# Performance work log

Hardware: AMD Instinct MI355X
Metric: run time of the kernel (lower is better)

The kernel has to match this reference:

```python
import jax, jax.numpy as jnp
import numpy as np

B, S, E, H = 4, 2048, 1024, 16
D = E // H  # head_size = 64


def setup_inputs() -> dict:
    key = jax.random.key(0)
    ks = jax.random.split(key, 8)
    s = 1.0 / np.sqrt(E)
    return {
        "values": jax.random.normal(ks[0], (B, S, E), jnp.float32),
        "keys": jax.random.normal(ks[1], (B, S, E), jnp.float32),
        "queries": jax.random.normal(ks[2], (B, S, E), jnp.float32),
        "Wv": jax.random.normal(ks[3], (E, E), jnp.float32) * s,
        "Wk": jax.random.normal(ks[4], (E, E), jnp.float32) * s,
        "Wq": jax.random.normal(ks[5], (E, E), jnp.float32) * s,
        "Wo": jax.random.normal(ks[6], (E, E), jnp.float32) * s,
        "bo": jax.random.normal(ks[7], (E,), jnp.float32) * s,
    }


def reference(values, keys, queries, Wv, Wk, Wq, Wo, bo):
    # torch Linear: y = x @ W.T
    k = (keys @ Wk.T).reshape(B, S, H, D).transpose(0, 2, 1, 3)    # [B,H,S,D]
    q = (queries @ Wq.T).reshape(B, S, H, D).transpose(0, 2, 1, 3)
    v = (values @ Wv.T).reshape(B, S, H, D).transpose(0, 2, 1, 3)
    dot = jnp.einsum('bhqd,bhkd->bhqk', q, k)                      # raw logits
    # NOTE: softmax BEFORE scaling (faithful to original module)
    probs = jax.nn.softmax(dot, axis=-1) / jnp.sqrt(jnp.float32(D))
    out = jnp.einsum('bhqk,bhkd->bhqd', probs, v)                  # [B,H,S,D]
    out = out.transpose(0, 2, 1, 3).reshape(B, S, E)
    return out @ Wo.T + bo
```

## Files before the change

### kernel.cpp

```cpp
#include <hip/hip_runtime.h>
#include <stdint.h>

#define NB 4
#define NS 2048
#define NE 1024
#define NH 16
#define ND 64

typedef __attribute__((ext_vector_type(8))) short short8;
typedef __attribute__((ext_vector_type(4))) float f32x4;
typedef __attribute__((ext_vector_type(16))) float f32x16;
typedef __attribute__((ext_vector_type(4))) unsigned short us4;
typedef __attribute__((ext_vector_type(4))) unsigned int u32x4;

__device__ __forceinline__ unsigned short f2bf(float f) {
    return __builtin_bit_cast(unsigned short, static_cast<__bf16>(f));
}
__device__ __forceinline__ unsigned int packbf(float lo, float hi_) {
    return (unsigned int)f2bf(lo) | ((unsigned int)f2bf(hi_) << 16);
}

__global__ __launch_bounds__(256) void cvt_w4_kernel(const float* __restrict__ w0,
                                                     const float* __restrict__ w1,
                                                     const float* __restrict__ w2,
                                                     const float* __restrict__ w3,
                                                     unsigned short* __restrict__ d0,
                                                     unsigned short* __restrict__ d1,
                                                     unsigned short* __restrict__ d2,
                                                     unsigned short* __restrict__ d3) {
    const int g = blockIdx.x >> 10;
    const float* src = g == 0 ? w0 : g == 1 ? w1 : g == 2 ? w2 : w3;
    unsigned short* dst = g == 0 ? d0 : g == 1 ? d1 : g == 2 ? d2 : d3;
    const int i = ((blockIdx.x & 1023) * 256 + threadIdx.x) * 4;
    f32x4 f = *(const f32x4*)(src + i);
    us4 o;
#pragma unroll
    for (int j = 0; j < 4; ++j) o[j] = f2bf(f[j]);
    *(us4*)(dst + i) = o;
}

template<int A_IS_F32, int OUT_MODE>
__global__ __launch_bounds__(256) void gemm_bt(const void* __restrict__ Aptr,
                                               const unsigned short* __restrict__ Wp,
                                               void* __restrict__ Cp,
                                               const float* __restrict__ bias) {
    constexpr int K = 1024;
    __shared__ unsigned short As[128][40];
    __shared__ unsigned short Bs[128][40];
    const int tid = threadIdx.x;
    const int bm = blockIdx.x, bn = blockIdx.y;
    const int lane = tid & 63, wid = tid >> 6;
    const int lr = lane & 15, lg = lane >> 4;
    const int wr = wid >> 1, wc = wid & 1;
    const int srow = tid >> 1, shalf = tid & 1;

    f32x4 acc[4][4];
#pragma unroll
    for (int a = 0; a < 4; ++a)
#pragma unroll
        for (int b = 0; b < 4; ++b) acc[a][b] = (f32x4){0.f, 0.f, 0.f, 0.f};

    const size_t arow = (size_t)(bm * 128 + srow) * K + shalf * 16;
    const size_t brow = (size_t)(bn * 128 + srow) * K + shalf * 16;
    const float*          apF = (const float*)Aptr + arow;
    const unsigned short* apH = (const unsigned short*)Aptr + arow;
    const unsigned short* bp  = Wp + brow;

    f32x4 pa0, pa1, pa2, pa3;
    short8 pah0, pah1, pb0, pb1;
    if (A_IS_F32) {
        pa0 = *(const f32x4*)(apF);
        pa1 = *(const f32x4*)(apF + 4);
        pa2 = *(const f32x4*)(apF + 8);
        pa3 = *(const f32x4*)(apF + 12);
    } else {
        pah0 = *(const short8*)(apH);
        pah1 = *(const short8*)(apH + 8);
    }
    pb0 = *(const short8*)(bp);
    pb1 = *(const short8*)(bp + 8);

    for (int k0 = 0; k0 < K; k0 += 32) {
        __syncthreads();
        if (A_IS_F32) {
            short8 p0, p1;
#pragma unroll
            for (int j = 0; j < 4; ++j) {
                p0[j]     = (short)f2bf(pa0[j]);
                p0[j + 4] = (short)f2bf(pa1[j]);
                p1[j]     = (short)f2bf(pa2[j]);
                p1[j + 4] = (short)f2bf(pa3[j]);
            }
            *(short8*)&As[srow][shalf * 16]     = p0;
            *(short8*)&As[srow][shalf * 16 + 8] = p1;
        } else {
            *(short8*)&As[srow][shalf * 16]     = pah0;
            *(short8*)&As[srow][shalf * 16 + 8] = pah1;
        }
        *(short8*)&Bs[srow][shalf * 16]     = pb0;
        *(short8*)&Bs[srow][shalf * 16 + 8] = pb1;
        __syncthreads();

        if (k0 + 32 < K) {
            const int kn = k0 + 32;
            if (A_IS_F32) {
                pa0 = *(const f32x4*)(apF + kn);
                pa1 = *(const f32x4*)(apF + kn + 4);
                pa2 = *(const f32x4*)(apF + kn + 8);
                pa3 = *(const f32x4*)(apF + kn + 12);
            } else {
                pah0 = *(const short8*)(apH + kn);
                pah1 = *(const short8*)(apH + kn + 8);
            }
            pb0 = *(const short8*)(bp + kn);
            pb1 = *(const short8*)(bp + kn + 8);
        }

        short8 af[4], bfr[4];
#pragma unroll
        for (int mi = 0; mi < 4; ++mi) af[mi]  = *(const short8*)&As[wr * 64 + mi * 16 + lr][lg * 8];
#pragma unroll
        for (int ni = 0; ni < 4; ++ni) bfr[ni] = *(const short8*)&Bs[wc * 64 + ni * 16 + lr][lg * 8];
#pragma unroll
        for (int mi = 0; mi < 4; ++mi)
#pragma unroll
            for (int ni = 0; ni < 4; ++ni)
                acc[mi][ni] = __builtin_amdgcn_mfma_f32_16x16x32_bf16(af[mi], bfr[ni], acc[mi][ni], 0, 0, 0);
    }

#pragma unroll
    for (int mi = 0; mi < 4; ++mi) {
#pragma unroll
        for (int ni = 0; ni < 4; ++ni) {
            const int n = bn * 128 + wc * 64 + ni * 16 + lr;
            if (OUT_MODE == 2) {
                const int m0 = bm * 128 + wr * 64 + mi * 16 + lg * 4;
                const int b = m0 >> 11, s0 = m0 & 2047;
                const int h = n >> 6, d = n & 63;
                us4 pk;
#pragma unroll
                for (int i = 0; i < 4; ++i) pk[i] = f2bf(acc[mi][ni][i]);
                const size_t idx = ((((size_t)b * NH + h) * (NS / 64) + (s0 >> 6)) * ND + d) * 64 + (s0 & 63);
                *(us4*)&((unsigned short*)Cp)[idx] = pk;
            } else {
#pragma unroll
                for (int i = 0; i < 4; ++i) {
                    const int m = bm * 128 + wr * 64 + mi * 16 + lg * 4 + i;
                    const float val = acc[mi][ni][i];
                    if (OUT_MODE == 0) {
                        const int b = m >> 11, s = m & 2047, h = n >> 6, d = n & 63;
                        ((unsigned short*)Cp)[(((size_t)b * NH + h) * NS + s) * ND + d] = f2bf(val);
                    } else {
                        ((float*)Cp)[(size_t)m * 1024 + n] = val + bias[n];
                    }
                }
            }
        }
    }
}

__global__ __launch_bounds__(256, 3) void attn_kernel(const unsigned short* __restrict__ q,
                                                      const unsigned short* __restrict__ k,
                                                      const unsigned short* __restrict__ vtt,
                                                      unsigned short* __restrict__ o) {
    __shared__ unsigned short Kl[64][72];
    __shared__ unsigned short Vl[64][72];
    const int tid = threadIdx.x;
    const int lane = tid & 63, wid = tid >> 6;
    const int l31 = lane & 31, hi = lane >> 5;
    const int bh = blockIdx.y;
    const int qw = blockIdx.x * 128 + wid * 32;
    const size_t base = (size_t)bh * NS * ND;

    short8 qf[4];
    {
        const unsigned short* qp = q + base + (size_t)(qw + l31) * ND + 8 * hi;
#pragma unroll
        for (int m = 0; m < 4; ++m) qf[m] = *(const short8*)(qp + 16 * m);
    }

    float m_run = -__builtin_inff(), l_run = 0.f;
    f32x16 oa0, oa1, fz;
#pragma unroll
    for (int i = 0; i < 16; ++i) { oa0[i] = 0.f; oa1[i] = 0.f; fz[i] = 0.f; }

    const int strow = tid >> 2, stcol = (tid & 3) * 16;
    const unsigned short* ks = k   + base + tid * 16;
    const unsigned short* vs = vtt + base + tid * 16;

    short8 kr0 = *(const short8*)(ks);
    short8 kr1 = *(const short8*)(ks + 8);
    short8 vr0 = *(const short8*)(vs);
    short8 vr1 = *(const short8*)(vs + 8);

    for (int kv0 = 0; kv0 < NS; kv0 += 64) {
        __syncthreads();
        *(short8*)&Kl[strow][stcol]     = kr0;
        *(short8*)&Kl[strow][stcol + 8] = kr1;
        *(short8*)&Vl[strow][stcol]     = vr0;
        *(short8*)&Vl[strow][stcol + 8] = vr1;
        __syncthreads();

        if (kv0 + 64 < NS) {
            const unsigned short* ks2 = ks + (size_t)(kv0 + 64) * ND;
            const unsigned short* vs2 = vs + (size_t)(kv0 + 64) * ND;
            kr0 = *(const short8*)(ks2);
            kr1 = *(const short8*)(ks2 + 8);
            vr0 = *(const short8*)(vs2);
            vr1 = *(const short8*)(vs2 + 8);
        }

        f32x16 st0, st1;
        __builtin_amdgcn_s_setprio(1);
        {
            short8 kf;
            kf = *(const short8*)&Kl[l31][8 * hi];
            st0 = __builtin_amdgcn_mfma_f32_32x32x16_bf16(kf, qf[0], fz, 0, 0, 0);
            kf = *(const short8*)&Kl[l31][16 + 8 * hi];
            st0 = __builtin_amdgcn_mfma_f32_32x32x16_bf16(kf, qf[1], st0, 0, 0, 0);
            kf = *(const short8*)&Kl[l31][32 + 8 * hi];
            st0 = __builtin_amdgcn_mfma_f32_32x32x16_bf16(kf, qf[2], st0, 0, 0, 0);
            kf = *(const short8*)&Kl[l31][48 + 8 * hi];
            st0 = __builtin_amdgcn_mfma_f32_32x32x16_bf16(kf, qf[3], st0, 0, 0, 0);
            kf = *(const short8*)&Kl[32 + l31][8 * hi];
            st1 = __builtin_amdgcn_mfma_f32_32x32x16_bf16(kf, qf[0], fz, 0, 0, 0);
            kf = *(const short8*)&Kl[32 + l31][16 + 8 * hi];
            st1 = __builtin_amdgcn_mfma_f32_32x32x16_bf16(kf, qf[1], st1, 0, 0, 0);
            kf = *(const short8*)&Kl[32 + l31][32 + 8 * hi];
            st1 = __builtin_amdgcn_mfma_f32_32x32x16_bf16(kf, qf[2], st1, 0, 0, 0);
            kf = *(const short8*)&Kl[32 + l31][48 + 8 * hi];
            st1 = __builtin_amdgcn_mfma_f32_32x32x16_bf16(kf, qf[3], st1, 0, 0, 0);
        }
        __builtin_amdgcn_s_setprio(0);

        float pm = st0[0];
#pragma unroll
        for (int i = 1; i < 16; ++i) pm = fmaxf(pm, st0[i]);
#pragma unroll
        for (int i = 0; i < 16; ++i) pm = fmaxf(pm, st1[i]);
        pm = fmaxf(pm, __shfl_xor(pm, 32, 64));
        if (!__all(pm <= m_run)) {
            const float mn = fmaxf(m_run, pm);
            const float alpha = __expf(m_run - mn);
            m_run = mn;
            l_run *= alpha;
#pragma unroll
            for (int i = 0; i < 16; ++i) { oa0[i] *= alpha; oa1[i] *= alpha; }
        }
        float rs = 0.f;
#pragma unroll
        for (int i = 0; i < 16; ++i) { st0[i] = __expf(st0[i] - m_run); rs += st0[i]; }
#pragma unroll
        for (int i = 0; i < 16; ++i) { st1[i] = __expf(st1[i] - m_run); rs += st1[i]; }
        rs += __shfl_xor(rs, 32, 64);
        l_run += rs;

        short8 pf0, pf1, pf2, pf3;
#define MKPF(PF, SV, RB) { \
        unsigned int wa = packbf(SV[RB + 0], SV[RB + 1]); \
        unsigned int wb = packbf(SV[RB + 2], SV[RB + 3]); \
        unsigned int wc = packbf(SV[RB + 4], SV[RB + 5]); \
        unsigned int wd = packbf(SV[RB + 6], SV[RB + 7]); \
        asm("v_permlane32_swap_b32 %0, %1" : "+v"(wa), "+v"(wc)); \
        asm("v_permlane32_swap_b32 %0, %1" : "+v"(wb), "+v"(wd)); \
        u32x4 pw; pw[0] = wa; pw[1] = wb; pw[2] = wc; pw[3] = wd; \
        PF = __builtin_bit_cast(short8, pw); }
        MKPF(pf0, st0, 0)
        MKPF(pf1, st0, 8)
        MKPF(pf2, st1, 0)
        MKPF(pf3, st1, 8)
#undef MKPF

        __builtin_amdgcn_s_setprio(1);
        {
            short8 vf;
            vf = *(const short8*)&Vl[l31][8 * hi];
            oa0 = __builtin_amdgcn_mfma_f32_32x32x16_bf16(vf, pf0, oa0, 0, 0, 0);
            vf = *(const short8*)&Vl[l31][16 + 8 * hi];
            oa0 = __builtin_amdgcn_mfma_f32_32x32x16_bf16(vf, pf1, oa0, 0, 0, 0);
            vf = *(const short8*)&Vl[l31][32 + 8 * hi];
            oa0 = __builtin_amdgcn_mfma_f32_32x32x16_bf16(vf, pf2, oa0, 0, 0, 0);
            vf = *(const short8*)&Vl[l31][48 + 8 * hi];
            oa0 = __builtin_amdgcn_mfma_f32_32x32x16_bf16(vf, pf3, oa0, 0, 0, 0);
            vf = *(const short8*)&Vl[32 + l31][8 * hi];
            oa1 = __builtin_amdgcn_mfma_f32_32x32x16_bf16(vf, pf0, oa1, 0, 0, 0);
            vf = *(const short8*)&Vl[32 + l31][16 + 8 * hi];
            oa1 = __builtin_amdgcn_mfma_f32_32x32x16_bf16(vf, pf1, oa1, 0, 0, 0);
            vf = *(const short8*)&Vl[32 + l31][32 + 8 * hi];
            oa1 = __builtin_amdgcn_mfma_f32_32x32x16_bf16(vf, pf2, oa1, 0, 0, 0);
            vf = *(const short8*)&Vl[32 + l31][48 + 8 * hi];
            oa1 = __builtin_amdgcn_mfma_f32_32x32x16_bf16(vf, pf3, oa1, 0, 0, 0);
        }
        __builtin_amdgcn_s_setprio(0);
    }

    const int b = bh >> 4, h = bh & 15;
    const float scl = 0.125f / l_run;
    unsigned short* op = o + (((size_t)b * NS + (qw + l31)) * NH + h) * ND;
#pragma unroll
    for (int rq = 0; rq < 4; ++rq) {
        us4 p0, p1;
#pragma unroll
        for (int i = 0; i < 4; ++i) {
            p0[i] = f2bf(oa0[4 * rq + i] * scl);
            p1[i] = f2bf(oa1[4 * rq + i] * scl);
        }
        *(us4*)&op[8 * rq + 4 * hi]      = p0;
        *(us4*)&op[32 + 8 * rq + 4 * hi] = p1;
    }
}

extern "C" void kernel_launch(void* const* d_in, const int* in_sizes, int n_in,
                              void* d_out, int out_size, void* d_ws, size_t ws_size,
                              hipStream_t stream) {
    (void)in_sizes; (void)n_in; (void)out_size; (void)ws_size;
    const float* values  = (const float*)d_in[0];
    const float* keys    = (const float*)d_in[1];
    const float* queries = (const float*)d_in[2];
    const float* Wv = (const float*)d_in[3];
    const float* Wk = (const float*)d_in[4];
    const float* Wq = (const float*)d_in[5];
    const float* Wo = (const float*)d_in[6];
    const float* bo = (const float*)d_in[7];

    uint8_t* ws = (uint8_t*)d_ws;
    const size_t MB = (size_t)1 << 20;
    unsigned short* wvb = (unsigned short*)(ws + 0 * MB);
    unsigned short* wkb = (unsigned short*)(ws + 2 * MB);
    unsigned short* wqb = (unsigned short*)(ws + 4 * MB);
    unsigned short* wob = (unsigned short*)(ws + 6 * MB);
    unsigned short* qb  = (unsigned short*)(ws + 8 * MB);
    unsigned short* kb  = (unsigned short*)(ws + 24 * MB);
    unsigned short* vtb = (unsigned short*)(ws + 40 * MB);
    unsigned short* ab  = (unsigned short*)(ws + 56 * MB);

    cvt_w4_kernel<<<4096, 256, 0, stream>>>(Wv, Wk, Wq, Wo, wvb, wkb, wqb, wob);

    dim3 gg(64, 8);
    gemm_bt<1, 0><<<gg, 256, 0, stream>>>(queries, wqb, qb,  nullptr);
    gemm_bt<1, 0><<<gg, 256, 0, stream>>>(keys,    wkb, kb,  nullptr);
    gemm_bt<1, 2><<<gg, 256, 0, stream>>>(values,  wvb, vtb, nullptr);

    attn_kernel<<<dim3(16, 64), 256, 0, stream>>>(qb, kb, vtb, ab);

    gemm_bt<0, 1><<<gg, 256, 0, stream>>>(ab, wob, d_out, bo);
}
```

Measured before the change: 245.5 us.

## Fold log2e into Wq, use exp2 softmax, and process 128-key tiles per barrier

The log2(e) factor is folded into the bf16 conversion of the query weight, so attention logits come out in base-2 and the softmax uses exp2f directly with no per-element multiply. The K/V staging tile grows from 64 to 128 keys, with two 64-key compute sub-steps per barrier pair, halving the number of syncs and giving the prefetch more time to land. The row-sum reduction becomes a tree of vector adds, and bf16 packing uses a vector convert that can lower to a packed conversion instruction. In exchange LDS use doubles and register pressure rises, which may reduce occupancy under the 3-block launch bound.

```diff
diff --git a/kernel.cpp b/kernel.cpp
--- a/kernel.cpp
+++ b/kernel.cpp
@@ -8,16 +8,22 @@
 #define ND 64
 
 typedef __attribute__((ext_vector_type(8))) short short8;
+typedef __attribute__((ext_vector_type(2))) float f32x2;
 typedef __attribute__((ext_vector_type(4))) float f32x4;
+typedef __attribute__((ext_vector_type(8))) float f32x8;
 typedef __attribute__((ext_vector_type(16))) float f32x16;
 typedef __attribute__((ext_vector_type(4))) unsigned short us4;
 typedef __attribute__((ext_vector_type(4))) unsigned int u32x4;
+typedef __attribute__((ext_vector_type(2))) __bf16 bf16x2;
+
+#define LOG2E 1.4426950408889634f
 
 __device__ __forceinline__ unsigned short f2bf(float f) {
     return __builtin_bit_cast(unsigned short, static_cast<__bf16>(f));
 }
 __device__ __forceinline__ unsigned int packbf(float lo, float hi_) {
-    return (unsigned int)f2bf(lo) | ((unsigned int)f2bf(hi_) << 16);
+    f32x2 v; v[0] = lo; v[1] = hi_;
+    return __builtin_bit_cast(unsigned int, __builtin_convertvector(v, bf16x2));
 }
 
 __global__ __launch_bounds__(256) void cvt_w4_kernel(const float* __restrict__ w0,
@@ -31,11 +37,12 @@
     const int g = blockIdx.x >> 10;
     const float* src = g == 0 ? w0 : g == 1 ? w1 : g == 2 ? w2 : w3;
     unsigned short* dst = g == 0 ? d0 : g == 1 ? d1 : g == 2 ? d2 : d3;
+    const float scl = (g == 2) ? LOG2E : 1.0f;
     const int i = ((blockIdx.x & 1023) * 256 + threadIdx.x) * 4;
     f32x4 f = *(const f32x4*)(src + i);
     us4 o;
 #pragma unroll
-    for (int j = 0; j < 4; ++j) o[j] = f2bf(f[j]);
+    for (int j = 0; j < 4; ++j) o[j] = f2bf(f[j] * scl);
     *(us4*)(dst + i) = o;
 }
 
@@ -163,8 +170,8 @@
                                                       const unsigned short* __restrict__ k,
                                                       const unsigned short* __restrict__ vtt,
                                                       unsigned short* __restrict__ o) {
-    __shared__ unsigned short Kl[64][72];
-    __shared__ unsigned short Vl[64][72];
+    __shared__ unsigned short Kl[128][72];
+    __shared__ unsigned short Vl[128][72];
     const int tid = threadIdx.x;
     const int lane = tid & 63, wid = tid >> 6;
     const int l31 = lane & 31, hi = lane >> 5;
@@ -188,110 +195,138 @@
     const unsigned short* ks = k   + base + tid * 16;
     const unsigned short* vs = vtt + base + tid * 16;
 
-    short8 kr0 = *(const short8*)(ks);
-    short8 kr1 = *(const short8*)(ks + 8);
-    short8 vr0 = *(const short8*)(vs);
-    short8 vr1 = *(const short8*)(vs + 8);
-
-    for (int kv0 = 0; kv0 < NS; kv0 += 64) {
+    short8 kr00 = *(const short8*)(ks);
+    short8 kr01 = *(const short8*)(ks + 8);
+    short8 kr10 = *(const short8*)(ks + 4096);
+    short8 kr11 = *(const short8*)(ks + 4096 + 8);
+    short8 vr00 = *(const short8*)(vs);
+    short8 vr01 = *(const short8*)(vs + 8);
+    short8 vr10 = *(const short8*)(vs + 4096);
+    short8 vr11 = *(const short8*)(vs + 4096 + 8);
+
+    for (int kv0 = 0; kv0 < NS; kv0 += 128) {
         __syncthreads();
-        *(short8*)&Kl[strow][stcol]     = kr0;
-        *(short8*)&Kl[strow][stcol + 8] = kr1;
-        *(short8*)&Vl[strow][stcol]     = vr0;
-        *(short8*)&Vl[strow][stcol + 8] = vr1;
+        *(short8*)&Kl[strow][stcol]          = kr00;
+        *(short8*)&Kl[strow][stcol + 8]      = kr01;
+        *(short8*)&Kl[64 + strow][stcol]     = kr10;
+        *(short8*)&Kl[64 + strow][stcol + 8] = kr11;
+        *(short8*)&Vl[strow][stcol]          = vr00;
+        *(short8*)&Vl[strow][stcol + 8]      = vr01;
+        *(short8*)&Vl[64 + strow][stcol]     = vr10;
+        *(short8*)&Vl[64 + strow][stcol + 8] = vr11;
         __syncthreads();
 
-        if (kv0 + 64 < NS) {
-            const unsigned short* ks2 = ks + (size_t)(kv0 + 64) * ND;
-            const unsigned short* vs2 = vs + (size_t)(kv0 + 64) * ND;
-            kr0 = *(const short8*)(ks2);
-            kr1 = *(const short8*)(ks2 + 8);
-            vr0 = *(const short8*)(vs2);
-            vr1 = *(const short8*)(vs2 + 8);
-        }
-
-        f32x16 st0, st1;
-        __builtin_amdgcn_s_setprio(1);
-        {
-            short8 kf;
-            kf = *(const short8*)&Kl[l31][8 * hi];
-            st0 = __builtin_amdgcn_mfma_f32_32x32x16_bf16(kf, qf[0], fz, 0, 0, 0);
-            kf = *(const short8*)&Kl[l31][16 + 8 * hi];
-            st0 = __builtin_amdgcn_mfma_f32_32x32x16_bf16(kf, qf[1], st0, 0, 0, 0);
-            kf = *(const short8*)&Kl[l31][32 + 8 * hi];
-            st0 = __builtin_amdgcn_mfma_f32_32x32x16_bf16(kf, qf[2], st0, 0, 0, 0);
-            kf = *(const short8*)&Kl[l31][48 + 8 * hi];
-            st0 = __builtin_amdgcn_mfma_f32_32x32x16_bf16(kf, qf[3], st0, 0, 0, 0);
-            kf = *(const short8*)&Kl[32 + l31][8 * hi];
-            st1 = __builtin_amdgcn_mfma_f32_32x32x16_bf16(kf, qf[0], fz, 0, 0, 0);
-            kf = *(const short8*)&Kl[32 + l31][16 + 8 * hi];
-            st1 = __builtin_amdgcn_mfma_f32_32x32x16_bf16(kf, qf[1], st1, 0, 0, 0);
-            kf = *(const short8*)&Kl[32 + l31][32 + 8 * hi];
-            st1 = __builtin_amdgcn_mfma_f32_32x32x16_bf16(kf, qf[2], st1, 0, 0, 0);
-            kf = *(const short8*)&Kl[32 + l31][48 + 8 * hi];
-            st1 = __builtin_amdgcn_mfma_f32_32x32x16_bf16(kf, qf[3], st1, 0, 0, 0);
-        }
-        __builtin_amdgcn_s_setprio(0);
-
-        float pm = st0[0];
-#pragma unroll
-        for (int i = 1; i < 16; ++i) pm = fmaxf(pm, st0[i]);
-#pragma unroll
-        for (int i = 0; i < 16; ++i) pm = fmaxf(pm, st1[i]);
-        pm = fmaxf(pm, __shfl_xor(pm, 32, 64));
-        if (!__all(pm <= m_run)) {
-            const float mn = fmaxf(m_run, pm);
-            const float alpha = __expf(m_run - mn);
-            m_run = mn;
-            l_run *= alpha;
-#pragma unroll
-            for (int i = 0; i < 16; ++i) { oa0[i] *= alpha; oa1[i] *= alpha; }
-        }
-        float rs = 0.f;
-#pragma unroll
-        for (int i = 0; i < 16; ++i) { st0[i] = __expf(st0[i] - m_run); rs += st0[i]; }
-#pragma unroll
-        for (int i = 0; i < 16; ++i) { st1[i] = __expf(st1[i] - m_run); rs += st1[i]; }
-        rs += __shfl_xor(rs, 32, 64);
-        l_run += rs;
-
-        short8 pf0, pf1, pf2, pf3;
+        if (kv0 + 128 < NS) {
+            const unsigned short* ks2 = ks + (size_t)(kv0 + 128) * ND;
+            const unsigned short* vs2 = vs + (size_t)(kv0 + 128) * ND;
+            kr00 = *(const short8*)(ks2);
+            kr01 = *(const short8*)(ks2 + 8);
+            kr10 = *(const short8*)(ks2 + 4096);
+            kr11 = *(const short8*)(ks2 + 4096 + 8);
+            vr00 = *(const short8*)(vs2);
+            vr01 = *(const short8*)(vs2 + 8);
+            vr10 = *(const short8*)(vs2 + 4096);
+            vr11 = *(const short8*)(vs2 + 4096 + 8);
+        }
+
+#pragma unroll
+        for (int w = 0; w < 2; ++w) {
+            const int rb = w << 6;
+
+            f32x16 st0, st1;
+            __builtin_amdgcn_s_setprio(1);
+            {
+                short8 kf;
+                kf = *(const short8*)&Kl[rb + l31][8 * hi];
+                st0 = __builtin_amdgcn_mfma_f32_32x32x16_bf16(kf, qf[0], fz, 0, 0, 0);
+                kf = *(const short8*)&Kl[rb + l31][16 + 8 * hi];
+                st0 = __builtin_amdgcn_mfma_f32_32x32x16_bf16(kf, qf[1], st0, 0, 0, 0);
+                kf = *(const short8*)&Kl[rb + l31][32 + 8 * hi];
+                st0 = __builtin_amdgcn_mfma_f32_32x32x16_bf16(kf, qf[2], st0, 0, 0, 0);
+                kf = *(const short8*)&Kl[rb + l31][48 + 8 * hi];
+                st0 = __builtin_amdgcn_mfma_f32_32x32x16_bf16(kf, qf[3], st0, 0, 0, 0);
+                kf = *(const short8*)&Kl[rb + 32 + l31][8 * hi];
+                st1 = __builtin_amdgcn_mfma_f32_32x32x16_bf16(kf, qf[0], fz, 0, 0, 0);
+                kf = *(const short8*)&Kl[rb + 32 + l31][16 + 8 * hi];
+                st1 = __builtin_amdgcn_mfma_f32_32x32x16_bf16(kf, qf[1], st1, 0, 0, 0);
+                kf = *(const short8*)&Kl[rb + 32 + l31][32 + 8 * hi];
+                st1 = __builtin_amdgcn_mfma_f32_32x32x16_bf16(kf, qf[2], st1, 0, 0, 0);
+                kf = *(const short8*)&Kl[rb + 32 + l31][48 + 8 * hi];
+                st1 = __builtin_amdgcn_mfma_f32_32x32x16_bf16(kf, qf[3], st1, 0, 0, 0);
+            }
+            __builtin_amdgcn_s_setprio(0);
+
+            float pm = st0[0];
+#pragma unroll
+            for (int i = 1; i < 16; ++i) pm = fmaxf(pm, st0[i]);
+#pragma unroll
+            for (int i = 0; i < 16; ++i) pm = fmaxf(pm, st1[i]);
+            pm = fmaxf(pm, __shfl_xor(pm, 32, 64));
+            if (!__all(pm <= m_run)) {
+                const float mn = fmaxf(m_run, pm);
+                const float alpha = exp2f(m_run - mn);
+                m_run = mn;
+                l_run *= alpha;
+                oa0 = oa0 * alpha;
+                oa1 = oa1 * alpha;
+            }
+            st0 = st0 - m_run;
+            st1 = st1 - m_run;
+#pragma unroll
+            for (int i = 0; i < 16; ++i) st0[i] = exp2f(st0[i]);
+#pragma unroll
+            for (int i = 0; i < 16; ++i) st1[i] = exp2f(st1[i]);
+            {
+                f32x16 sv = st0 + st1;
+                f32x8 s8 = __builtin_shufflevector(sv, sv, 0, 1, 2, 3, 4, 5, 6, 7)
+                         + __builtin_shufflevector(sv, sv, 8, 9, 10, 11, 12, 13, 14, 15);
+                f32x4 s4 = __builtin_shufflevector(s8, s8, 0, 1, 2, 3)
+                         + __builtin_shufflevector(s8, s8, 4, 5, 6, 7);
+                f32x2 s2 = __builtin_shufflevector(s4, s4, 0, 1)
+                         + __builtin_shufflevector(s4, s4, 2, 3);
+                float rs = s2[0] + s2[1];
+                rs += __shfl_xor(rs, 32, 64);
+                l_run += rs;
+            }
+
+            short8 pf0, pf1, pf2, pf3;
 #define MKPF(PF, SV, RB) { \
-        unsigned int wa = packbf(SV[RB + 0], SV[RB + 1]); \
-        unsigned int wb = packbf(SV[RB + 2], SV[RB + 3]); \
-        unsigned int wc = packbf(SV[RB + 4], SV[RB + 5]); \
-        unsigned int wd = packbf(SV[RB + 6], SV[RB + 7]); \
-        asm("v_permlane32_swap_b32 %0, %1" : "+v"(wa), "+v"(wc)); \
-        asm("v_permlane32_swap_b32 %0, %1" : "+v"(wb), "+v"(wd)); \
-        u32x4 pw; pw[0] = wa; pw[1] = wb; pw[2] = wc; pw[3] = wd; \
-        PF = __builtin_bit_cast(short8, pw); }
-        MKPF(pf0, st0, 0)
-        MKPF(pf1, st0, 8)
-        MKPF(pf2, st1, 0)
-        MKPF(pf3, st1, 8)
+            unsigned int wa = packbf(SV[RB + 0], SV[RB + 1]); \
+            unsigned int wb = packbf(SV[RB + 2], SV[RB + 3]); \
+            unsigned int wc = packbf(SV[RB + 4], SV[RB + 5]); \
+            unsigned int wd = packbf(SV[RB + 6], SV[RB + 7]); \
+            asm("v_permlane32_swap_b32 %0, %1" : "+v"(wa), "+v"(wc)); \
+            asm("v_permlane32_swap_b32 %0, %1" : "+v"(wb), "+v"(wd)); \
+            u32x4 pw; pw[0] = wa; pw[1] = wb; pw[2] = wc; pw[3] = wd; \
+            PF = __builtin_bit_cast(short8, pw); }
+            MKPF(pf0, st0, 0)
+            MKPF(pf1, st0, 8)
+            MKPF(pf2, st1, 0)
+            MKPF(pf3, st1, 8)
 #undef MKPF
 
-        __builtin_amdgcn_s_setprio(1);
-        {
-            short8 vf;
-            vf = *(const short8*)&Vl[l31][8 * hi];
-            oa0 = __builtin_amdgcn_mfma_f32_32x32x16_bf16(vf, pf0, oa0, 0, 0, 0);
-            vf = *(const short8*)&Vl[l31][16 + 8 * hi];
-            oa0 = __builtin_amdgcn_mfma_f32_32x32x16_bf16(vf, pf1, oa0, 0, 0, 0);
-            vf = *(const short8*)&Vl[l31][32 + 8 * hi];
-            oa0 = __builtin_amdgcn_mfma_f32_32x32x16_bf16(vf, pf2, oa0, 0, 0, 0);
-            vf = *(const short8*)&Vl[l31][48 + 8 * hi];
-            oa0 = __builtin_amdgcn_mfma_f32_32x32x16_bf16(vf, pf3, oa0, 0, 0, 0);
-            vf = *(const short8*)&Vl[32 + l31][8 * hi];
-            oa1 = __builtin_amdgcn_mfma_f32_32x32x16_bf16(vf, pf0, oa1, 0, 0, 0);
-            vf = *(const short8*)&Vl[32 + l31][16 + 8 * hi];
-            oa1 = __builtin_amdgcn_mfma_f32_32x32x16_bf16(vf, pf1, oa1, 0, 0, 0);
-            vf = *(const short8*)&Vl[32 + l31][32 + 8 * hi];
-            oa1 = __builtin_amdgcn_mfma_f32_32x32x16_bf16(vf, pf2, oa1, 0, 0, 0);
-            vf = *(const short8*)&Vl[32 + l31][48 + 8 * hi];
-            oa1 = __builtin_amdgcn_mfma_f32_32x32x16_bf16(vf, pf3, oa1, 0, 0, 0);
-        }
-        __builtin_amdgcn_s_setprio(0);
+            __builtin_amdgcn_s_setprio(1);
+            {
+                short8 vf;
+                vf = *(const short8*)&Vl[rb + l31][8 * hi];
+                oa0 = __builtin_amdgcn_mfma_f32_32x32x16_bf16(vf, pf0, oa0, 0, 0, 0);
+                vf = *(const short8*)&Vl[rb + l31][16 + 8 * hi];
+                oa0 = __builtin_amdgcn_mfma_f32_32x32x16_bf16(vf, pf1, oa0, 0, 0, 0);
+                vf = *(const short8*)&Vl[rb + l31][32 + 8 * hi];
+                oa0 = __builtin_amdgcn_mfma_f32_32x32x16_bf16(vf, pf2, oa0, 0, 0, 0);
+                vf = *(const short8*)&Vl[rb + l31][48 + 8 * hi];
+                oa0 = __builtin_amdgcn_mfma_f32_32x32x16_bf16(vf, pf3, oa0, 0, 0, 0);
+                vf = *(const short8*)&Vl[rb + 32 + l31][8 * hi];
+                oa1 = __builtin_amdgcn_mfma_f32_32x32x16_bf16(vf, pf0, oa1, 0, 0, 0);
+                vf = *(const short8*)&Vl[rb + 32 + l31][16 + 8 * hi];
+                oa1 = __builtin_amdgcn_mfma_f32_32x32x16_bf16(vf, pf1, oa1, 0, 0, 0);
+                vf = *(const short8*)&Vl[rb + 32 + l31][32 + 8 * hi];
+                oa1 = __builtin_amdgcn_mfma_f32_32x32x16_bf16(vf, pf2, oa1, 0, 0, 0);
+                vf = *(const short8*)&Vl[rb + 32 + l31][48 + 8 * hi];
+                oa1 = __builtin_amdgcn_mfma_f32_32x32x16_bf16(vf, pf3, oa1, 0, 0, 0);
+            }
+            __builtin_amdgcn_s_setprio(0);
+        }
     }
 
     const int b = bh >> 4, h = bh & 15;
```

Result: slower. 254.6 us (+3.7%).

## Fold log2e into Wq, use exp2 softmax, packed bf16 convert, raise occupancy

Applied to the files above, without the earlier changes.

Pre-scales the query projection weight by log2(e) during bf16 conversion so attention can use exp2f directly instead of __expf, which drops a multiply per exponent. It also switches the bf16 pair packing to a vector convert that can map to a packed conversion instruction, vectorizes the subtract and row-sum with a tree reduction for packed float ops, and raises launch_bounds min blocks from 3 to 4. Folding log2e into the weights changes bf16 rounding of Q slightly. The higher occupancy target may force register spills.

```diff
diff --git a/kernel.cpp b/kernel.cpp
--- a/kernel.cpp
+++ b/kernel.cpp
@@ -8,16 +8,22 @@
 #define ND 64
 
 typedef __attribute__((ext_vector_type(8))) short short8;
+typedef __attribute__((ext_vector_type(2))) float f32x2;
 typedef __attribute__((ext_vector_type(4))) float f32x4;
+typedef __attribute__((ext_vector_type(8))) float f32x8;
 typedef __attribute__((ext_vector_type(16))) float f32x16;
 typedef __attribute__((ext_vector_type(4))) unsigned short us4;
 typedef __attribute__((ext_vector_type(4))) unsigned int u32x4;
+typedef __attribute__((ext_vector_type(2))) __bf16 bf16x2;
+
+#define LOG2E 1.4426950408889634f
 
 __device__ __forceinline__ unsigned short f2bf(float f) {
     return __builtin_bit_cast(unsigned short, static_cast<__bf16>(f));
 }
 __device__ __forceinline__ unsigned int packbf(float lo, float hi_) {
-    return (unsigned int)f2bf(lo) | ((unsigned int)f2bf(hi_) << 16);
+    f32x2 v; v[0] = lo; v[1] = hi_;
+    return __builtin_bit_cast(unsigned int, __builtin_convertvector(v, bf16x2));
 }
 
 __global__ __launch_bounds__(256) void cvt_w4_kernel(const float* __restrict__ w0,
@@ -31,11 +37,12 @@
     const int g = blockIdx.x >> 10;
     const float* src = g == 0 ? w0 : g == 1 ? w1 : g == 2 ? w2 : w3;
     unsigned short* dst = g == 0 ? d0 : g == 1 ? d1 : g == 2 ? d2 : d3;
+    const float scl = (g == 2) ? LOG2E : 1.0f;
     const int i = ((blockIdx.x & 1023) * 256 + threadIdx.x) * 4;
     f32x4 f = *(const f32x4*)(src + i);
     us4 o;
 #pragma unroll
-    for (int j = 0; j < 4; ++j) o[j] = f2bf(f[j]);
+    for (int j = 0; j < 4; ++j) o[j] = f2bf(f[j] * scl);
     *(us4*)(dst + i) = o;
 }
 
@@ -159,7 +166,7 @@
     }
 }
 
-__global__ __launch_bounds__(256, 3) void attn_kernel(const unsigned short* __restrict__ q,
+__global__ __launch_bounds__(256, 4) void attn_kernel(const unsigned short* __restrict__ q,
                                                       const unsigned short* __restrict__ k,
                                                       const unsigned short* __restrict__ vtt,
                                                       unsigned short* __restrict__ o) {
@@ -241,19 +248,30 @@
         pm = fmaxf(pm, __shfl_xor(pm, 32, 64));
         if (!__all(pm <= m_run)) {
             const float mn = fmaxf(m_run, pm);
-            const float alpha = __expf(m_run - mn);
+            const float alpha = exp2f(m_run - mn);
             m_run = mn;
             l_run *= alpha;
-#pragma unroll
-            for (int i = 0; i < 16; ++i) { oa0[i] *= alpha; oa1[i] *= alpha; }
-        }
-        float rs = 0.f;
-#pragma unroll
-        for (int i = 0; i < 16; ++i) { st0[i] = __expf(st0[i] - m_run); rs += st0[i]; }
-#pragma unroll
-        for (int i = 0; i < 16; ++i) { st1[i] = __expf(st1[i] - m_run); rs += st1[i]; }
-        rs += __shfl_xor(rs, 32, 64);
-        l_run += rs;
+            oa0 = oa0 * alpha;
+            oa1 = oa1 * alpha;
+        }
+        st0 = st0 - m_run;
+        st1 = st1 - m_run;
+#pragma unroll
+        for (int i = 0; i < 16; ++i) st0[i] = exp2f(st0[i]);
+#pragma unroll
+        for (int i = 0; i < 16; ++i) st1[i] = exp2f(st1[i]);
+        {
+            f32x16 sv = st0 + st1;
+            f32x8 s8 = __builtin_shufflevector(sv, sv, 0, 1, 2, 3, 4, 5, 6, 7)
+                     + __builtin_shufflevector(sv, sv, 8, 9, 10, 11, 12, 13, 14, 15);
+            f32x4 s4 = __builtin_shufflevector(s8, s8, 0, 1, 2, 3)
+                     + __builtin_shufflevector(s8, s8, 4, 5, 6, 7);
+            f32x2 s2 = __builtin_shufflevector(s4, s4, 0, 1)
+                     + __builtin_shufflevector(s4, s4, 2, 3);
+            float rs = s2[0] + s2[1];
+            rs += __shfl_xor(rs, 32, 64);
+            l_run += rs;
+        }
 
         short8 pf0, pf1, pf2, pf3;
 #define MKPF(PF, SV, RB) { \
```

Result: slower. 257.8 us (+5.0%).
